# Kernel optimization log

Hardware: AMD Instinct MI355X
Metric: run time of the kernel (lower is better)

The kernel has to match this reference:

```python
import jax, jax.numpy as jnp
import numpy as np

B, N, D, CF = 8, 2048, 512, 128  # batch, nodes, feat_dim, count_feat


def setup_inputs() -> dict:
    key = jax.random.key(0)
    ks = jax.random.split(key, 12)
    s = 1.0 / np.sqrt(D)
    return {
        "X": jax.random.normal(ks[0], (B, N, D), jnp.float32),
        # first MultiHeadAttention (num_heads=1, mode='QK', out_features=feat_dim)
        "Wq1": jax.random.normal(ks[1], (D, D), jnp.float32) * s,
        "Wk1": jax.random.normal(ks[2], (D, D), jnp.float32) * s,
        "Wv1": jax.random.normal(ks[3], (D, D), jnp.float32) * s,
        "Wo1": jax.random.normal(ks[4], (D, D), jnp.float32) * s,
        # score attention (only its raw QK^T scores are used downstream)
        "Wq2": jax.random.normal(ks[5], (D, D), jnp.float32) * s,
        "Wk2": jax.random.normal(ks[6], (D, D), jnp.float32) * s,
        # count_mlp: Linear(D,CF) -> LeakyReLU(0.1) -> Linear(CF,1)
        "W1": jax.random.normal(ks[7], (D, CF), jnp.float32) * s,
        "b1": jnp.zeros((CF,), jnp.float32),
        "W2": jax.random.normal(ks[8], (CF, 1), jnp.float32) * (1.0 / np.sqrt(CF)),
        "b2": jnp.zeros((1,), jnp.float32),
    }


def reference(X, Wq1, Wk1, Wv1, Wo1, Wq2, Wk2, W1, b1, W2, b2):
    scale = 1.0 / jnp.sqrt(jnp.asarray(X.shape[-1], X.dtype))
    # --- first self-attention: att = softmax(QK^T/sqrt(d)) V Wo ---
    q1 = X @ Wq1
    k1 = X @ Wk1
    v1 = X @ Wv1
    s1 = jnp.einsum("bnd,bmd->bnm", q1, k1) * scale      # [B,N,N]
    p1 = jax.nn.softmax(s1, axis=-1)
    att = jnp.einsum("bnm,bmd->bnd", p1, v1) @ Wo1        # [B,N,D]
    # --- score attention over att: only raw scores are consumed ---
    s2 = jnp.einsum("bnd,bmd->bnm", att @ Wq2, att @ Wk2) * scale  # [B,N,N]
    # --- count_mlp threshold per node ---
    h = att @ W1 + b1
    h = jnp.where(h >= 0, h, 0.1 * h)                     # LeakyReLU(0.1)
    thresh = h @ W2 + b2                                  # [B,N,1]
    # --- mlp_score_thresh readout: clamp, row-normalize, clip ---
    surv = jnp.maximum(s2 - thresh, 0.0)                  # broadcast over last dim
    A = jnp.clip(surv / (jnp.sum(surv, axis=-1, keepdims=True) + 1e-9), 0.0, 1.0)
    return A
```

## Files before the change

### kernel.cpp

```cpp
#include <hip/hip_runtime.h>
#include <hip/hip_bf16.h>

#define BB 8
#define NN 2048
#define DD 512
#define CFF 128
#define MT (BB*NN)

typedef _Float16 half_t;
typedef __attribute__((ext_vector_type(8))) _Float16 half8;
typedef __attribute__((ext_vector_type(4))) float floatx4;
typedef __attribute__((ext_vector_type(4))) unsigned int uint4v;

#define MFMA16(a,b,c) __builtin_amdgcn_mfma_f32_16x16x32_f16((a),(b),(c),0,0,0)

template<int EPI>
__global__ __launch_bounds__(256) void gemm_f16s(
    const half_t* __restrict__ Ahi, const half_t* __restrict__ Alo, long lda, long sA,
    const half_t* __restrict__ Bhi, const half_t* __restrict__ Blo, long ldb, long sB,
    float* __restrict__ Cf, half_t* __restrict__ Chi, half_t* __restrict__ Clo,
    long ldc, long sC, long slotS,
    int K, float alpha, const float* __restrict__ bias, const float* __restrict__ tvec,
    float* __restrict__ rsum)
{
    const int gx = gridDim.x, gy = gridDim.y;
    int d = blockIdx.x + gx * (blockIdx.y + gy * blockIdx.z);
    int total = gx * gy * gridDim.z;
    int t0 = (d & 7) * (total >> 3) + (d >> 3);
    int bx = t0 % gx;
    int t1 = t0 / gx;
    int by = t1 % gy;
    int bz = t1 / gy;

    const int tid = threadIdx.x;
    const int row0 = by * 128, col0 = bx * 128;
    const long z = bz;
    const half_t* pAh = Ahi + z * sA + (long)row0 * lda;
    const half_t* pAl = Alo + z * sA + (long)row0 * lda;
    const half_t* pBh = Bhi + z * sB + (long)col0 * ldb;
    const half_t* pBl = Blo + z * sB + (long)col0 * ldb;

    __shared__ half_t lds[2][4][4096];

    const int l  = tid & 63;
    const int w  = tid >> 6;
    const int wr = w >> 1, wc = w & 1;
    const int Rw = wr * 64, Cw = wc * 64;
    const int rl = l & 15, kc = l >> 4;
    const int swz = (kc ^ ((rl >> 1) & 3)) * 8;

    floatx4 acc[4][4];
#pragma unroll
    for (int m = 0; m < 4; ++m)
#pragma unroll
        for (int n = 0; n < 4; ++n) acc[m][n] = (floatx4){0.f, 0.f, 0.f, 0.f};

    const int r0s = tid >> 2,         c0s = tid & 3;
    const int r1s = (tid + 256) >> 2, c1s = tid & 3;
    const int off0 = r0s * 32 + ((c0s ^ ((r0s >> 1) & 3)) * 8);
    const int off1 = r1s * 32 + ((c1s ^ ((r1s >> 1) & 3)) * 8);

    auto load_regs = [&](int k0, uint4v* r) {
        long ga0 = (long)r0s * lda + k0 + c0s * 8;
        long gb0 = (long)r0s * ldb + k0 + c0s * 8;
        long ga1 = (long)r1s * lda + k0 + c1s * 8;
        long gb1 = (long)r1s * ldb + k0 + c1s * 8;
        r[0] = *(const uint4v*)(pAh + ga0);
        r[1] = *(const uint4v*)(pAl + ga0);
        r[2] = *(const uint4v*)(pBh + gb0);
        r[3] = *(const uint4v*)(pBl + gb0);
        r[4] = *(const uint4v*)(pAh + ga1);
        r[5] = *(const uint4v*)(pAl + ga1);
        r[6] = *(const uint4v*)(pBh + gb1);
        r[7] = *(const uint4v*)(pBl + gb1);
    };
    auto write_lds = [&](int buf, const uint4v* r) {
        *(uint4v*)&lds[buf][0][off0] = r[0];
        *(uint4v*)&lds[buf][1][off0] = r[1];
        *(uint4v*)&lds[buf][2][off0] = r[2];
        *(uint4v*)&lds[buf][3][off0] = r[3];
        *(uint4v*)&lds[buf][0][off1] = r[4];
        *(uint4v*)&lds[buf][1][off1] = r[5];
        *(uint4v*)&lds[buf][2][off1] = r[6];
        *(uint4v*)&lds[buf][3][off1] = r[7];
    };

    const int nk = K >> 5;
    uint4v rg[8];
    load_regs(0, rg);
    write_lds(0, rg);
#pragma unroll 2
    for (int t = 0; t < nk; ++t) {
        __syncthreads();
        if (t + 1 < nk) load_regs((t + 1) << 5, rg);
        const int cur = t & 1;
        const half_t* bAh = &lds[cur][0][0];
        const half_t* bAl = &lds[cur][1][0];
        const half_t* bBh = &lds[cur][2][0];
        const half_t* bBl = &lds[cur][3][0];
        half8 af[4][2], bf[4][2];
#pragma unroll
        for (int m = 0; m < 4; ++m) {
            int off = (Rw + m * 16 + rl) * 32 + swz;
            af[m][0] = *(const half8*)(bAh + off);
            af[m][1] = *(const half8*)(bAl + off);
        }
#pragma unroll
        for (int n = 0; n < 4; ++n) {
            int off = (Cw + n * 16 + rl) * 32 + swz;
            bf[n][0] = *(const half8*)(bBh + off);
            bf[n][1] = *(const half8*)(bBl + off);
        }
        __builtin_amdgcn_s_setprio(1);
#pragma unroll
        for (int m = 0; m < 4; ++m)
#pragma unroll
            for (int n = 0; n < 4; ++n) {
                acc[m][n] = MFMA16(af[m][0], bf[n][0], acc[m][n]);
                acc[m][n] = MFMA16(af[m][1], bf[n][0], acc[m][n]);
                acc[m][n] = MFMA16(af[m][0], bf[n][1], acc[m][n]);
            }
        __builtin_amdgcn_s_setprio(0);
        if (t + 1 < nk) write_lds((t + 1) & 1, rg);
    }

    if (EPI == 0) {
#pragma unroll
        for (int m = 0; m < 4; ++m)
#pragma unroll
            for (int n = 0; n < 4; ++n) {
                int col = col0 + Cw + n * 16 + rl;
#pragma unroll
                for (int r = 0; r < 4; ++r) {
                    int row = row0 + Rw + m * 16 + kc * 4 + r;
                    Cf[z * sC + (long)row * ldc + col] = acc[m][n][r] * alpha;
                }
            }
    } else if (EPI == 1) {
#pragma unroll
        for (int m = 0; m < 4; ++m)
#pragma unroll
            for (int n = 0; n < 4; ++n) {
                int col = col0 + Cw + n * 16 + rl;
                long obase = (long)(col >> 9) * slotS + z * sC + (col & 511);
#pragma unroll
                for (int r = 0; r < 4; ++r) {
                    int row = row0 + Rw + m * 16 + kc * 4 + r;
                    long o = obase + (long)row * ldc;
                    float v = acc[m][n][r] * alpha;
                    half_t hh = (half_t)v;
                    Chi[o] = hh;
                    Clo[o] = (half_t)(v - (float)hh);
                }
            }
    } else if (EPI == 3) {
        const float* tv = tvec + z * NN;
        float* rs = rsum + z * NN;
#pragma unroll
        for (int m = 0; m < 4; ++m) {
#pragma unroll
            for (int r = 0; r < 4; ++r) {
                int row = row0 + Rw + m * 16 + kc * 4 + r;
                float tvr = tv[row];
                float partial = 0.f;
#pragma unroll
                for (int n = 0; n < 4; ++n) {
                    int col = col0 + Cw + n * 16 + rl;
                    float v = fmaxf(acc[m][n][r] * alpha - tvr, 0.f);
                    Cf[z * sC + (long)row * ldc + col] = v;
                    partial += v;
                }
                partial += __shfl_xor(partial, 1);
                partial += __shfl_xor(partial, 2);
                partial += __shfl_xor(partial, 4);
                partial += __shfl_xor(partial, 8);
                if (rl == 0) atomicAdd(&rs[row], partial);
            }
        }
    } else {
        float w2v[4], bv[4];
#pragma unroll
        for (int n = 0; n < 4; ++n) {
            int col = Cw + n * 16 + rl;
            bv[n]  = bias[col];
            w2v[n] = tvec[col];
        }
#pragma unroll
        for (int m = 0; m < 4; ++m) {
#pragma unroll
            for (int r = 0; r < 4; ++r) {
                int row = row0 + Rw + m * 16 + kc * 4 + r;
                float partial = 0.f;
#pragma unroll
                for (int n = 0; n < 4; ++n) {
                    float v = acc[m][n][r] + bv[n];
                    v = (v >= 0.f) ? v : 0.1f * v;
                    partial += v * w2v[n];
                }
                partial += __shfl_xor(partial, 1);
                partial += __shfl_xor(partial, 2);
                partial += __shfl_xor(partial, 4);
                partial += __shfl_xor(partial, 8);
                if (rl == 0) atomicAdd(&rsum[row], partial);
            }
        }
    }
}

__global__ __launch_bounds__(256) void wgemm3(
    const float* __restrict__ Wq1, const float* __restrict__ Wk1,
    const float* __restrict__ Wv1, const float* __restrict__ Wo1,
    const float* __restrict__ Wq2, const float* __restrict__ Wk2,
    float* __restrict__ T0, float* __restrict__ T1, float* __restrict__ T2)
{
    const int op = blockIdx.z;
    const float* A = (op == 0) ? Wq1 : (op == 1) ? Wv1 : Wq2;
    const float* B = (op == 0) ? Wk1 : (op == 1) ? Wo1 : Wk2;
    float* C = (op == 0) ? T0 : (op == 1) ? T1 : T2;
    const bool bt = (op != 1);

    __shared__ float As[32][65];
    __shared__ float Bs[32][65];
    const int tid = threadIdx.x;
    const int i0 = blockIdx.y * 64, j0 = blockIdx.x * 64;
    const int tx = tid & 15, ty = tid >> 4;
    float acc[4][4];
#pragma unroll
    for (int i = 0; i < 4; ++i)
#pragma unroll
        for (int j = 0; j < 4; ++j) acc[i][j] = 0.f;

    for (int k0 = 0; k0 < 512; k0 += 32) {
#pragma unroll
        for (int u = 0; u < 2; ++u) {
            int e = tid + u * 256;
            int r = e >> 3, c = (e & 7) * 4;
            float4 v = *(const float4*)(A + (long)(i0 + r) * 512 + k0 + c);
            As[c][r] = v.x; As[c + 1][r] = v.y; As[c + 2][r] = v.z; As[c + 3][r] = v.w;
        }
        if (bt) {
#pragma unroll
            for (int u = 0; u < 2; ++u) {
                int e = tid + u * 256;
                int r = e >> 3, c = (e & 7) * 4;
                float4 v = *(const float4*)(B + (long)(j0 + r) * 512 + k0 + c);
                Bs[c][r] = v.x; Bs[c + 1][r] = v.y; Bs[c + 2][r] = v.z; Bs[c + 3][r] = v.w;
            }
        } else {
#pragma unroll
            for (int u = 0; u < 2; ++u) {
                int e = tid + u * 256;
                int k = e >> 4, j = (e & 15) * 4;
                *(float4*)&Bs[k][j] = *(const float4*)(B + (long)(k0 + k) * 512 + j0 + j);
            }
        }
        __syncthreads();
#pragma unroll
        for (int kk = 0; kk < 32; ++kk) {
            float av[4], bv[4];
#pragma unroll
            for (int i = 0; i < 4; ++i) av[i] = As[kk][ty * 4 + i];
#pragma unroll
            for (int j = 0; j < 4; ++j) bv[j] = Bs[kk][tx * 4 + j];
#pragma unroll
            for (int i = 0; i < 4; ++i)
#pragma unroll
                for (int j = 0; j < 4; ++j)
                    acc[i][j] = fmaf(av[i], bv[j], acc[i][j]);
        }
        __syncthreads();
    }
#pragma unroll
    for (int i = 0; i < 4; ++i)
#pragma unroll
        for (int j = 0; j < 4; ++j)
            C[(long)(i0 + ty * 4 + i) * 512 + j0 + tx * 4 + j] = acc[i][j];
}

__device__ __forceinline__ float waveReduceMax(float v) {
#pragma unroll
    for (int o = 32; o; o >>= 1) v = fmaxf(v, __shfl_down(v, o));
    return v;
}
__device__ __forceinline__ float waveReduceSum(float v) {
#pragma unroll
    for (int o = 32; o; o >>= 1) v += __shfl_down(v, o);
    return v;
}

__global__ __launch_bounds__(256) void softmax_split_kernel(float* __restrict__ S)
{
    __shared__ float red[4];
    __shared__ float fin;
    long row = blockIdx.x;
    float* p = S + row * (long)NN;
    half_t* ph = (half_t*)p;
    half_t* pl = ph + NN;
    int t = threadIdx.x;

    float4 v0 = *reinterpret_cast<float4*>(p + t * 8);
    float4 v1 = *reinterpret_cast<float4*>(p + t * 8 + 4);

    float m = fmaxf(fmaxf(fmaxf(v0.x, v0.y), fmaxf(v0.z, v0.w)),
                    fmaxf(fmaxf(v1.x, v1.y), fmaxf(v1.z, v1.w)));
    m = waveReduceMax(m);
    if ((t & 63) == 0) red[t >> 6] = m;
    __syncthreads();
    if (t == 0) fin = fmaxf(fmaxf(red[0], red[1]), fmaxf(red[2], red[3]));
    __syncthreads();
    m = fin;

    float e[8];
    e[0] = __expf(v0.x - m); e[1] = __expf(v0.y - m); e[2] = __expf(v0.z - m); e[3] = __expf(v0.w - m);
    e[4] = __expf(v1.x - m); e[5] = __expf(v1.y - m); e[6] = __expf(v1.z - m); e[7] = __expf(v1.w - m);
    float s = ((e[0] + e[1]) + (e[2] + e[3])) + ((e[4] + e[5]) + (e[6] + e[7]));
    s = waveReduceSum(s);
    __syncthreads();
    if ((t & 63) == 0) red[t >> 6] = s;
    __syncthreads();
    if (t == 0) fin = (red[0] + red[1]) + (red[2] + red[3]);
    __syncthreads();
    float inv = 1.0f / fin;

    __syncthreads();
    half8 hv, lv;
#pragma unroll
    for (int j = 0; j < 8; ++j) {
        float pv = e[j] * inv;
        half_t hh = (half_t)pv;
        hv[j] = hh;
        lv[j] = (half_t)(pv - (float)hh);
    }
    *(half8*)(ph + t * 8) = hv;
    *(half8*)(pl + t * 8) = lv;
}

__global__ __launch_bounds__(256) void norm_kernel(float* __restrict__ S, const float* __restrict__ sums)
{
    long i = (long)blockIdx.x * 256 + threadIdx.x;
    long base = i * 8;
    long row = base >> 11;
    float inv = 1.0f / (sums[row] + 1e-9f);
    float4 v0 = *reinterpret_cast<float4*>(S + base);
    float4 v1 = *reinterpret_cast<float4*>(S + base + 4);
    v0.x = fminf(v0.x * inv, 1.0f); v0.y = fminf(v0.y * inv, 1.0f);
    v0.z = fminf(v0.z * inv, 1.0f); v0.w = fminf(v0.w * inv, 1.0f);
    v1.x = fminf(v1.x * inv, 1.0f); v1.y = fminf(v1.y * inv, 1.0f);
    v1.z = fminf(v1.z * inv, 1.0f); v1.w = fminf(v1.w * inv, 1.0f);
    *reinterpret_cast<float4*>(S + base) = v0;
    *reinterpret_cast<float4*>(S + base + 4) = v1;
}

__global__ __launch_bounds__(256) void init_aux(float* __restrict__ thresh, float* __restrict__ sums,
                                                const float* __restrict__ b2)
{
    int i = blockIdx.x * 256 + threadIdx.x;
    if (i < MT) { thresh[i] = b2[0]; sums[i] = 0.f; }
}

__global__ __launch_bounds__(256) void wprep(const float* __restrict__ W,
                                             half_t* __restrict__ Th, half_t* __restrict__ Tl,
                                             int K, int N, float mul)
{
    __shared__ float tw[32][33];
    int n0 = blockIdx.x * 32, k0 = blockIdx.y * 32;
    int c = threadIdx.x & 31, r8 = threadIdx.x >> 5;
#pragma unroll
    for (int i = 0; i < 4; ++i) {
        int r = r8 + i * 8;
        tw[r][c] = W[(long)(k0 + r) * N + n0 + c];
    }
    __syncthreads();
#pragma unroll
    for (int i = 0; i < 4; ++i) {
        int nr = r8 + i * 8;
        float v = tw[c][nr] * mul;
        half_t hh = (half_t)v;
        Th[(long)(n0 + nr) * K + k0 + c] = hh;
        Tl[(long)(n0 + nr) * K + k0 + c] = (half_t)(v - (float)hh);
    }
}

__global__ __launch_bounds__(256) void split_f32(const float* __restrict__ in,
                                                 half_t* __restrict__ hi, half_t* __restrict__ lo)
{
    long i = ((long)blockIdx.x * 256 + threadIdx.x) * 8;
    float4 a = *(const float4*)(in + i), b = *(const float4*)(in + i + 4);
    float v[8] = {a.x, a.y, a.z, a.w, b.x, b.y, b.z, b.w};
    half8 hv, lv;
#pragma unroll
    for (int j = 0; j < 8; ++j) {
        half_t hh = (half_t)v[j];
        hv[j] = hh;
        lv[j] = (half_t)(v[j] - (float)hh);
    }
    *(half8*)(hi + i) = hv;
    *(half8*)(lo + i) = lv;
}

static void launch_gemm16(hipStream_t s, int epi,
    const half_t* Ahi, const half_t* Alo, long lda, long sA,
    const half_t* Bhi, const half_t* Blo, long ldb, long sB,
    float* Cf, half_t* Chi, half_t* Clo, long ldc, long sC, long slotS,
    int M, int N, int K, int batch, float alpha,
    const float* bias, const float* tvec, float* rsum)
{
    dim3 g(N / 128, M / 128, batch), b(256, 1, 1);
    if (epi == 0)      gemm_f16s<0><<<g, b, 0, s>>>(Ahi, Alo, lda, sA, Bhi, Blo, ldb, sB, Cf, Chi, Clo, ldc, sC, slotS, K, alpha, bias, tvec, rsum);
    else if (epi == 1) gemm_f16s<1><<<g, b, 0, s>>>(Ahi, Alo, lda, sA, Bhi, Blo, ldb, sB, Cf, Chi, Clo, ldc, sC, slotS, K, alpha, bias, tvec, rsum);
    else if (epi == 3) gemm_f16s<3><<<g, b, 0, s>>>(Ahi, Alo, lda, sA, Bhi, Blo, ldb, sB, Cf, Chi, Clo, ldc, sC, slotS, K, alpha, bias, tvec, rsum);
    else               gemm_f16s<4><<<g, b, 0, s>>>(Ahi, Alo, lda, sA, Bhi, Blo, ldb, sB, Cf, Chi, Clo, ldc, sC, slotS, K, alpha, bias, tvec, rsum);
}

extern "C" void kernel_launch(void* const* d_in, const int* in_sizes, int n_in,
                              void* d_out, int out_size, void* d_ws, size_t ws_size,
                              hipStream_t stream)
{
    const float* X   = (const float*)d_in[0];
    const float* Wq1 = (const float*)d_in[1];
    const float* Wk1 = (const float*)d_in[2];
    const float* Wv1 = (const float*)d_in[3];
    const float* Wo1 = (const float*)d_in[4];
    const float* Wq2 = (const float*)d_in[5];
    const float* Wk2 = (const float*)d_in[6];
    const float* W1  = (const float*)d_in[7];
    const float* b1  = (const float*)d_in[8];
    const float* W2  = (const float*)d_in[9];
    const float* b2  = (const float*)d_in[10];

    float* out = (float*)d_out;
    const float scale = 0.044194173824159216f;
    const float WM = 8.0f, WMI = 0.125f;

    half_t* wsH = (half_t*)d_ws;
    const long U  = (long)MT * DD;
    const long WD = (long)DD * DD;
    half_t* sXh = wsH;          half_t* sXl = wsH + U;
    half_t* sBh = wsH + 2 * U;  half_t* sBl = wsH + 3 * U;
    half_t* sCh = wsH + 4 * U;  half_t* sCl = wsH + 5 * U;
    half_t* wptr = wsH + 6 * U;
    half_t* mb1h = wptr;            half_t* mb1l = mb1h + WD;
    half_t* mvoh = mb1l + WD;       half_t* mvol = mvoh + WD;
    half_t* mb2h = mvol + WD;       half_t* mb2l = mb2h + WD;
    half_t* w1h  = mb2l + WD;       half_t* w1l  = w1h + (long)DD * CFF;
    float*  T0 = (float*)(w1l + (long)DD * CFF);
    float*  T1 = T0 + WD;
    float*  T2 = T1 + WD;
    float*  thresh = T2 + WD;
    float*  sums   = thresh + MT;

    init_aux<<<dim3(64), dim3(256), 0, stream>>>(thresh, sums, b2);
    split_f32<<<dim3(4096), dim3(256), 0, stream>>>(X, sXh, sXl);
    wgemm3<<<dim3(8, 8, 3), dim3(256), 0, stream>>>(Wq1, Wk1, Wv1, Wo1, Wq2, Wk2, T0, T1, T2);
    wprep<<<dim3(16, 16), dim3(256), 0, stream>>>(T0, mb1h, mb1l, DD, DD, WM);
    wprep<<<dim3(16, 16), dim3(256), 0, stream>>>(T1, mvoh, mvol, DD, DD, WM);
    wprep<<<dim3(16, 16), dim3(256), 0, stream>>>(T2, mb2h, mb2l, DD, DD, WM);
    wprep<<<dim3(4, 16),  dim3(256), 0, stream>>>(W1, w1h, w1l, DD, CFF, 1.0f);

    launch_gemm16(stream, 1, sXh, sXl, DD, 0, mb1h, mb1l, DD, 0,
                  nullptr, sBh, sBl, DD, 0, 0, MT, DD, DD, 1, WMI, nullptr, nullptr, nullptr);

    launch_gemm16(stream, 0, sBh, sBl, DD, (long)NN * DD, sXh, sXl, DD, (long)NN * DD,
                  out, nullptr, nullptr, NN, (long)NN * NN, 0, NN, NN, DD, BB, scale, nullptr, nullptr, nullptr);

    launch_gemm16(stream, 1, mvoh, mvol, DD, 0, sXh, sXl, DD, (long)NN * DD,
                  nullptr, sBh, sBl, NN, (long)DD * NN, 512, DD, NN, DD, BB, WMI, nullptr, nullptr, nullptr);

    softmax_split_kernel<<<dim3(MT), dim3(256), 0, stream>>>(out);

    {
        const half_t* p1h = (const half_t*)d_out;
        const half_t* p1l = p1h + NN;
        launch_gemm16(stream, 1, p1h, p1l, 2 * NN, (long)NN * 2 * NN,
                      sBh, sBl, NN, (long)DD * NN,
                      nullptr, sCh, sCl, DD, (long)NN * DD, 0, NN, DD, NN, BB, 1.f, nullptr, nullptr, nullptr);
    }

    launch_gemm16(stream, 1, sCh, sCl, DD, 0, mb2h, mb2l, DD, 0,
                  nullptr, sBh, sBl, DD, 0, 0, MT, DD, DD, 1, WMI, nullptr, nullptr, nullptr);

    launch_gemm16(stream, 4, sCh, sCl, DD, 0, w1h, w1l, DD, 0,
                  nullptr, nullptr, nullptr, CFF, 0, 0, MT, CFF, DD, 1, 1.f, b1, W2, thresh);

    launch_gemm16(stream, 3, sBh, sBl, DD, (long)NN * DD, sCh, sCl, DD, (long)NN * DD,
                  out, nullptr, nullptr, NN, (long)NN * NN, 0, NN, NN, DD, BB, scale, nullptr, thresh, sums);

    norm_kernel<<<dim3(out_size / 2048), dim3(256), 0, stream>>>(out, sums);
}
```

Before: 728.1 us.

## Add 256-wide 512-thread split-f16 GEMM with XCD-aware block remap

Adds a new split-fp16 MFMA GEMM kernel using 256x256 (or 128x256) tiles, 8 waves, and a large dynamic-LDS double buffer. It also adds a block-index remap that spreads consecutive tiles across the 8 chiplet partitions. A dedicated GEMM handles the count-MLP threshold with the same remap. Every large GEMM is routed to the new kernels when the device reports at least 128KB of shared memory per block, to raise operand reuse per LDS load. In exchange the kernel uses far more registers and LDS, which limits occupancy to about one block per CU and can expose more load latency.

```diff
diff --git a/kernel.cpp b/kernel.cpp
--- a/kernel.cpp
+++ b/kernel.cpp
@@ -207,6 +207,320 @@
     }
 }
 
+template<int MF, int EPI>
+__global__ __launch_bounds__(512, 2) void gemm256(
+    const half_t* __restrict__ Ahi, const half_t* __restrict__ Alo, long lda, long sA,
+    const half_t* __restrict__ Bhi, const half_t* __restrict__ Blo, long ldb, long sB,
+    float* __restrict__ Cf, half_t* __restrict__ Chi, half_t* __restrict__ Clo,
+    long ldc, long sC, long slotS,
+    int K, float alpha, const float* __restrict__ tvec, float* __restrict__ rsum)
+{
+    constexpr int BM    = MF * 32;
+    constexpr int ATILE = BM * 32;
+    constexpr int BTILE = 256 * 32;
+    constexpr int PERBUF = 2 * ATILE + 2 * BTILE;
+    constexpr int oAh = 0, oAl = ATILE, oBh = 2 * ATILE, oBl = 2 * ATILE + BTILE;
+    constexpr int RA = (MF == 8) ? 2 : 1;
+
+    extern __shared__ half_t lds[];
+
+    const int gx = gridDim.x, gy = gridDim.y;
+    int d = blockIdx.x + gx * (blockIdx.y + gy * blockIdx.z);
+    int total = gx * gy * gridDim.z;
+    int t0 = (d & 7) * (total >> 3) + (d >> 3);
+    int bx = t0 % gx;
+    int t1 = t0 / gx;
+    int by = t1 % gy;
+    int bz = t1 / gy;
+
+    const int tid = threadIdx.x;
+    const int row0 = by * BM, col0 = bx * 256;
+    const long z = bz;
+    const half_t* pAh = Ahi + z * sA + (long)row0 * lda;
+    const half_t* pAl = Alo + z * sA + (long)row0 * lda;
+    const half_t* pBh = Bhi + z * sB + (long)col0 * ldb;
+    const half_t* pBl = Blo + z * sB + (long)col0 * ldb;
+
+    const int l  = tid & 63;
+    const int w  = tid >> 6;
+    const int wr = w >> 2, wc = w & 3;
+    const int Rw = wr * (BM / 2), Cw = wc * 64;
+    const int rl = l & 15, kc = l >> 4;
+    const int swz = (kc ^ ((rl >> 1) & 3)) * 8;
+
+    floatx4 acc[MF][4];
+#pragma unroll
+    for (int m = 0; m < MF; ++m)
+#pragma unroll
+        for (int n = 0; n < 4; ++n) acc[m][n] = (floatx4){0.f, 0.f, 0.f, 0.f};
+
+    long goffA[RA]; int loffA[RA];
+    long goffB[2];  int loffB[2];
+#pragma unroll
+    for (int u = 0; u < RA; ++u) {
+        int s = tid + u * 512; int r = s >> 2; int g = s & 3; int p = g ^ ((r >> 1) & 3);
+        goffA[u] = (long)r * lda + g * 8; loffA[u] = r * 32 + p * 8;
+    }
+#pragma unroll
+    for (int u = 0; u < 2; ++u) {
+        int s = tid + u * 512; int r = s >> 2; int g = s & 3; int p = g ^ ((r >> 1) & 3);
+        goffB[u] = (long)r * ldb + g * 8; loffB[u] = r * 32 + p * 8;
+    }
+
+    uint4v rgA[RA][2], rgB[2][2];
+    auto load_regs = [&](int k0) {
+#pragma unroll
+        for (int u = 0; u < RA; ++u) {
+            rgA[u][0] = *(const uint4v*)(pAh + goffA[u] + k0);
+            rgA[u][1] = *(const uint4v*)(pAl + goffA[u] + k0);
+        }
+#pragma unroll
+        for (int u = 0; u < 2; ++u) {
+            rgB[u][0] = *(const uint4v*)(pBh + goffB[u] + k0);
+            rgB[u][1] = *(const uint4v*)(pBl + goffB[u] + k0);
+        }
+    };
+    auto write_lds = [&](int buf) {
+        half_t* bp = lds + buf * PERBUF;
+#pragma unroll
+        for (int u = 0; u < RA; ++u) {
+            *(uint4v*)&bp[oAh + loffA[u]] = rgA[u][0];
+            *(uint4v*)&bp[oAl + loffA[u]] = rgA[u][1];
+        }
+#pragma unroll
+        for (int u = 0; u < 2; ++u) {
+            *(uint4v*)&bp[oBh + loffB[u]] = rgB[u][0];
+            *(uint4v*)&bp[oBl + loffB[u]] = rgB[u][1];
+        }
+    };
+
+    const int nk = K >> 5;
+    load_regs(0);
+    write_lds(0);
+#pragma unroll 2
+    for (int t = 0; t < nk; ++t) {
+        __syncthreads();
+        if (t + 1 < nk) load_regs((t + 1) << 5);
+        const half_t* bp = lds + (t & 1) * PERBUF;
+        half8 bf[4][2];
+#pragma unroll
+        for (int n = 0; n < 4; ++n) {
+            int off = (Cw + n * 16 + rl) * 32 + swz;
+            bf[n][0] = *(const half8*)(bp + oBh + off);
+            bf[n][1] = *(const half8*)(bp + oBl + off);
+        }
+#pragma unroll
+        for (int mp = 0; mp < MF / 2; ++mp) {
+            half8 af[2][2];
+#pragma unroll
+            for (int i = 0; i < 2; ++i) {
+                int off = (Rw + (mp * 2 + i) * 16 + rl) * 32 + swz;
+                af[i][0] = *(const half8*)(bp + oAh + off);
+                af[i][1] = *(const half8*)(bp + oAl + off);
+            }
+            __builtin_amdgcn_s_setprio(1);
+#pragma unroll
+            for (int i = 0; i < 2; ++i)
+#pragma unroll
+                for (int n = 0; n < 4; ++n) {
+                    const int m = mp * 2 + i;
+                    acc[m][n] = MFMA16(af[i][0], bf[n][0], acc[m][n]);
+                    acc[m][n] = MFMA16(af[i][1], bf[n][0], acc[m][n]);
+                    acc[m][n] = MFMA16(af[i][0], bf[n][1], acc[m][n]);
+                }
+            __builtin_amdgcn_s_setprio(0);
+        }
+        if (t + 1 < nk) write_lds((t + 1) & 1);
+    }
+
+    if (EPI == 0) {
+#pragma unroll
+        for (int m = 0; m < MF; ++m)
+#pragma unroll
+            for (int n = 0; n < 4; ++n) {
+                int col = col0 + Cw + n * 16 + rl;
+#pragma unroll
+                for (int r = 0; r < 4; ++r) {
+                    int row = row0 + Rw + m * 16 + kc * 4 + r;
+                    Cf[z * sC + (long)row * ldc + col] = acc[m][n][r] * alpha;
+                }
+            }
+    } else if (EPI == 1) {
+#pragma unroll
+        for (int m = 0; m < MF; ++m)
+#pragma unroll
+            for (int n = 0; n < 4; ++n) {
+                int col = col0 + Cw + n * 16 + rl;
+                long obase = (long)(col >> 9) * slotS + z * sC + (col & 511);
+#pragma unroll
+                for (int r = 0; r < 4; ++r) {
+                    int row = row0 + Rw + m * 16 + kc * 4 + r;
+                    long o = obase + (long)row * ldc;
+                    float v = acc[m][n][r] * alpha;
+                    half_t hh = (half_t)v;
+                    Chi[o] = hh;
+                    Clo[o] = (half_t)(v - (float)hh);
+                }
+            }
+    } else {
+        const float* tv = tvec + z * NN;
+        float* rs = rsum + z * NN;
+#pragma unroll
+        for (int m = 0; m < MF; ++m) {
+#pragma unroll
+            for (int r = 0; r < 4; ++r) {
+                int row = row0 + Rw + m * 16 + kc * 4 + r;
+                float tvr = tv[row];
+                float partial = 0.f;
+#pragma unroll
+                for (int n = 0; n < 4; ++n) {
+                    int col = col0 + Cw + n * 16 + rl;
+                    float v = fmaxf(acc[m][n][r] * alpha - tvr, 0.f);
+                    Cf[z * sC + (long)row * ldc + col] = v;
+                    partial += v;
+                }
+                partial += __shfl_xor(partial, 1);
+                partial += __shfl_xor(partial, 2);
+                partial += __shfl_xor(partial, 4);
+                partial += __shfl_xor(partial, 8);
+                if (rl == 0) atomicAdd(&rs[row], partial);
+            }
+        }
+    }
+}
+
+__global__ __launch_bounds__(256) void gemm_h(
+    const half_t* __restrict__ Ahi, const half_t* __restrict__ Alo, long lda,
+    const half_t* __restrict__ Bhi, const half_t* __restrict__ Blo, long ldb,
+    int K, const float* __restrict__ bias, const float* __restrict__ tvec,
+    float* __restrict__ rsum)
+{
+    const int gx = gridDim.x, gy = gridDim.y;
+    int d = blockIdx.x + gx * blockIdx.y;
+    int total = gx * gy;
+    int t0 = (d & 7) * (total >> 3) + (d >> 3);
+    int bx = t0 % gx;
+    int by = t0 / gx;
+
+    const int tid = threadIdx.x;
+    const int row0 = by * 128, col0 = bx * 128;
+    const half_t* pAh = Ahi + (long)row0 * lda;
+    const half_t* pAl = Alo + (long)row0 * lda;
+    const half_t* pBh = Bhi + (long)col0 * ldb;
+    const half_t* pBl = Blo + (long)col0 * ldb;
+
+    __shared__ half_t lds[2][4][4096];
+
+    const int l  = tid & 63;
+    const int w  = tid >> 6;
+    const int wr = w >> 1, wc = w & 1;
+    const int Rw = wr * 64, Cw = wc * 64;
+    const int rl = l & 15, kc = l >> 4;
+    const int swz = (kc ^ ((rl >> 1) & 3)) * 8;
+
+    floatx4 acc[4][4];
+#pragma unroll
+    for (int m = 0; m < 4; ++m)
+#pragma unroll
+        for (int n = 0; n < 4; ++n) acc[m][n] = (floatx4){0.f, 0.f, 0.f, 0.f};
+
+    const int r0s = tid >> 2,         c0s = tid & 3;
+    const int r1s = (tid + 256) >> 2, c1s = tid & 3;
+    const int off0 = r0s * 32 + ((c0s ^ ((r0s >> 1) & 3)) * 8);
+    const int off1 = r1s * 32 + ((c1s ^ ((r1s >> 1) & 3)) * 8);
+
+    auto load_regs = [&](int k0, uint4v* r) {
+        long ga0 = (long)r0s * lda + k0 + c0s * 8;
+        long gb0 = (long)r0s * ldb + k0 + c0s * 8;
+        long ga1 = (long)r1s * lda + k0 + c1s * 8;
+        long gb1 = (long)r1s * ldb + k0 + c1s * 8;
+        r[0] = *(const uint4v*)(pAh + ga0);
+        r[1] = *(const uint4v*)(pAl + ga0);
+        r[2] = *(const uint4v*)(pBh + gb0);
+        r[3] = *(const uint4v*)(pBl + gb0);
+        r[4] = *(const uint4v*)(pAh + ga1);
+        r[5] = *(const uint4v*)(pAl + ga1);
+        r[6] = *(const uint4v*)(pBh + gb1);
+        r[7] = *(const uint4v*)(pBl + gb1);
+    };
+    auto write_lds = [&](int buf, const uint4v* r) {
+        *(uint4v*)&lds[buf][0][off0] = r[0];
+        *(uint4v*)&lds[buf][1][off0] = r[1];
+        *(uint4v*)&lds[buf][2][off0] = r[2];
+        *(uint4v*)&lds[buf][3][off0] = r[3];
+        *(uint4v*)&lds[buf][0][off1] = r[4];
+        *(uint4v*)&lds[buf][1][off1] = r[5];
+        *(uint4v*)&lds[buf][2][off1] = r[6];
+        *(uint4v*)&lds[buf][3][off1] = r[7];
+    };
+
+    const int nk = K >> 5;
+    uint4v rg[8];
+    load_regs(0, rg);
+    write_lds(0, rg);
+#pragma unroll 2
+    for (int t = 0; t < nk; ++t) {
+        __syncthreads();
+        if (t + 1 < nk) load_regs((t + 1) << 5, rg);
+        const int cur = t & 1;
+        const half_t* bAh = &lds[cur][0][0];
+        const half_t* bAl = &lds[cur][1][0];
+        const half_t* bBh = &lds[cur][2][0];
+        const half_t* bBl = &lds[cur][3][0];
+        half8 af[4][2], bf[4][2];
+#pragma unroll
+        for (int m = 0; m < 4; ++m) {
+            int off = (Rw + m * 16 + rl) * 32 + swz;
+            af[m][0] = *(const half8*)(bAh + off);
+            af[m][1] = *(const half8*)(bAl + off);
+        }
+#pragma unroll
+        for (int n = 0; n < 4; ++n) {
+            int off = (Cw + n * 16 + rl) * 32 + swz;
+            bf[n][0] = *(const half8*)(bBh + off);
+            bf[n][1] = *(const half8*)(bBl + off);
+        }
+        __builtin_amdgcn_s_setprio(1);
+#pragma unroll
+        for (int m = 0; m < 4; ++m)
+#pragma unroll
+            for (int n = 0; n < 4; ++n) {
+                acc[m][n] = MFMA16(af[m][0], bf[n][0], acc[m][n]);
+                acc[m][n] = MFMA16(af[m][1], bf[n][0], acc[m][n]);
+                acc[m][n] = MFMA16(af[m][0], bf[n][1], acc[m][n]);
+            }
+        __builtin_amdgcn_s_setprio(0);
+        if (t + 1 < nk) write_lds((t + 1) & 1, rg);
+    }
+
+    float w2v[4], bv[4];
+#pragma unroll
+    for (int n = 0; n < 4; ++n) {
+        int col = Cw + n * 16 + rl;
+        bv[n]  = bias[col];
+        w2v[n] = tvec[col];
+    }
+#pragma unroll
+    for (int m = 0; m < 4; ++m) {
+#pragma unroll
+        for (int r = 0; r < 4; ++r) {
+            int row = row0 + Rw + m * 16 + kc * 4 + r;
+            float partial = 0.f;
+#pragma unroll
+            for (int n = 0; n < 4; ++n) {
+                float v = acc[m][n][r] + bv[n];
+                v = (v >= 0.f) ? v : 0.1f * v;
+                partial += v * w2v[n];
+            }
+            partial += __shfl_xor(partial, 1);
+            partial += __shfl_xor(partial, 2);
+            partial += __shfl_xor(partial, 4);
+            partial += __shfl_xor(partial, 8);
+            if (rl == 0) atomicAdd(&rsum[row], partial);
+        }
+    }
+}
+
 __global__ __launch_bounds__(256) void wgemm3(
     const float* __restrict__ Wq1, const float* __restrict__ Wk1,
     const float* __restrict__ Wv1, const float* __restrict__ Wo1,
@@ -412,6 +726,27 @@
     else               gemm_f16s<4><<<g, b, 0, s>>>(Ahi, Alo, lda, sA, Bhi, Blo, ldb, sB, Cf, Chi, Clo, ldc, sC, slotS, K, alpha, bias, tvec, rsum);
 }
 
+static void launch_g256(hipStream_t s, int mf, int epi,
+    const half_t* Ahi, const half_t* Alo, long lda, long sA,
+    const half_t* Bhi, const half_t* Blo, long ldb, long sB,
+    float* Cf, half_t* Chi, half_t* Clo, long ldc, long sC, long slotS,
+    int M, int N, int K, int batch, float alpha,
+    const float* tvec, float* rsum)
+{
+    dim3 b(512, 1, 1);
+    if (mf == 8) {
+        dim3 g(N / 256, M / 256, batch);
+        const size_t sh = 131072;
+        if (epi == 0)      gemm256<8, 0><<<g, b, sh, s>>>(Ahi, Alo, lda, sA, Bhi, Blo, ldb, sB, Cf, Chi, Clo, ldc, sC, slotS, K, alpha, tvec, rsum);
+        else if (epi == 1) gemm256<8, 1><<<g, b, sh, s>>>(Ahi, Alo, lda, sA, Bhi, Blo, ldb, sB, Cf, Chi, Clo, ldc, sC, slotS, K, alpha, tvec, rsum);
+        else               gemm256<8, 3><<<g, b, sh, s>>>(Ahi, Alo, lda, sA, Bhi, Blo, ldb, sB, Cf, Chi, Clo, ldc, sC, slotS, K, alpha, tvec, rsum);
+    } else {
+        dim3 g(N / 256, M / 128, batch);
+        const size_t sh = 98304;
+        gemm256<4, 1><<<g, b, sh, s>>>(Ahi, Alo, lda, sA, Bhi, Blo, ldb, sB, Cf, Chi, Clo, ldc, sC, slotS, K, alpha, tvec, rsum);
+    }
+}
+
 extern "C" void kernel_launch(void* const* d_in, const int* in_sizes, int n_in,
                               void* d_out, int out_size, void* d_ws, size_t ws_size,
                               hipStream_t stream)
@@ -431,6 +766,12 @@
     float* out = (float*)d_out;
     const float scale = 0.044194173824159216f;
     const float WM = 8.0f, WMI = 0.125f;
+
+    int dev = 0;
+    hipGetDevice(&dev);
+    int maxSh = 0;
+    hipDeviceGetAttribute(&maxSh, hipDeviceAttributeMaxSharedMemoryPerBlock, dev);
+    const bool big = (maxSh >= 131072);
 
     half_t* wsH = (half_t*)d_ws;
     const long U  = (long)MT * DD;
@@ -457,33 +798,46 @@
     wprep<<<dim3(16, 16), dim3(256), 0, stream>>>(T2, mb2h, mb2l, DD, DD, WM);
     wprep<<<dim3(4, 16),  dim3(256), 0, stream>>>(W1, w1h, w1l, DD, CFF, 1.0f);
 
-    launch_gemm16(stream, 1, sXh, sXl, DD, 0, mb1h, mb1l, DD, 0,
-                  nullptr, sBh, sBl, DD, 0, 0, MT, DD, DD, 1, WMI, nullptr, nullptr, nullptr);
-
-    launch_gemm16(stream, 0, sBh, sBl, DD, (long)NN * DD, sXh, sXl, DD, (long)NN * DD,
-                  out, nullptr, nullptr, NN, (long)NN * NN, 0, NN, NN, DD, BB, scale, nullptr, nullptr, nullptr);
-
-    launch_gemm16(stream, 1, mvoh, mvol, DD, 0, sXh, sXl, DD, (long)NN * DD,
-                  nullptr, sBh, sBl, NN, (long)DD * NN, 512, DD, NN, DD, BB, WMI, nullptr, nullptr, nullptr);
-
-    softmax_split_kernel<<<dim3(MT), dim3(256), 0, stream>>>(out);
-
-    {
-        const half_t* p1h = (const half_t*)d_out;
-        const half_t* p1l = p1h + NN;
+    const half_t* p1h = (const half_t*)d_out;
+    const half_t* p1l = p1h + NN;
+
+    if (big) {
+        launch_g256(stream, 8, 1, sXh, sXl, DD, 0, mb1h, mb1l, DD, 0,
+                    nullptr, sBh, sBl, DD, 0, 0, MT, DD, DD, 1, WMI, nullptr, nullptr);
+        launch_g256(stream, 8, 0, sBh, sBl, DD, (long)NN * DD, sXh, sXl, DD, (long)NN * DD,
+                    out, nullptr, nullptr, NN, (long)NN * NN, 0, NN, NN, DD, BB, scale, nullptr, nullptr);
+        launch_g256(stream, 8, 1, mvoh, mvol, DD, 0, sXh, sXl, DD, (long)NN * DD,
+                    nullptr, sBh, sBl, NN, (long)DD * NN, 512, DD, NN, DD, BB, WMI, nullptr, nullptr);
+        softmax_split_kernel<<<dim3(MT), dim3(256), 0, stream>>>(out);
+        launch_g256(stream, 4, 1, p1h, p1l, 2 * NN, (long)NN * 2 * NN,
+                    sBh, sBl, NN, (long)DD * NN,
+                    nullptr, sCh, sCl, DD, (long)NN * DD, 0, NN, DD, NN, BB, 1.f, nullptr, nullptr);
+        launch_g256(stream, 8, 1, sCh, sCl, DD, 0, mb2h, mb2l, DD, 0,
+                    nullptr, sBh, sBl, DD, 0, 0, MT, DD, DD, 1, WMI, nullptr, nullptr);
+        {
+            dim3 g(CFF / 128, MT / 128), b(256, 1, 1);
+            gemm_h<<<g, b, 0, stream>>>(sCh, sCl, DD, w1h, w1l, DD, DD, b1, W2, thresh);
+        }
+        launch_g256(stream, 8, 3, sBh, sBl, DD, (long)NN * DD, sCh, sCl, DD, (long)NN * DD,
+                    out, nullptr, nullptr, NN, (long)NN * NN, 0, NN, NN, DD, BB, scale, thresh, sums);
+    } else {
+        launch_gemm16(stream, 1, sXh, sXl, DD, 0, mb1h, mb1l, DD, 0,
+                      nullptr, sBh, sBl, DD, 0, 0, MT, DD, DD, 1, WMI, nullptr, nullptr, nullptr);
+        launch_gemm16(stream, 0, sBh, sBl, DD, (long)NN * DD, sXh, sXl, DD, (long)NN * DD,
+                      out, nullptr, nullptr, NN, (long)NN * NN, 0, NN, NN, DD, BB, scale, nullptr, nullptr, nullptr);
+        launch_gemm16(stream, 1, mvoh, mvol, DD, 0, sXh, sXl, DD, (long)NN * DD,
+                      nullptr, sBh, sBl, NN, (long)DD * NN, 512, DD, NN, DD, BB, WMI, nullptr, nullptr, nullptr);
+        softmax_split_kernel<<<dim3(MT), dim3(256), 0, stream>>>(out);
         launch_gemm16(stream, 1, p1h, p1l, 2 * NN, (long)NN * 2 * NN,
                       sBh, sBl, NN, (long)DD * NN,
                       nullptr, sCh, sCl, DD, (long)NN * DD, 0, NN, DD, NN, BB, 1.f, nullptr, nullptr, nullptr);
-    }
-
-    launch_gemm16(stream, 1, sCh, sCl, DD, 0, mb2h, mb2l, DD, 0,
-                  nullptr, sBh, sBl, DD, 0, 0, MT, DD, DD, 1, WMI, nullptr, nullptr, nullptr);
-
-    launch_gemm16(stream, 4, sCh, sCl, DD, 0, w1h, w1l, DD, 0,
-                  nullptr, nullptr, nullptr, CFF, 0, 0, MT, CFF, DD, 1, 1.f, b1, W2, thresh);
-
-    launch_gemm16(stream, 3, sBh, sBl, DD, (long)NN * DD, sCh, sCl, DD, (long)NN * DD,
-                  out, nullptr, nullptr, NN, (long)NN * NN, 0, NN, NN, DD, BB, scale, nullptr, thresh, sums);
+        launch_gemm16(stream, 1, sCh, sCl, DD, 0, mb2h, mb2l, DD, 0,
+                      nullptr, sBh, sBl, DD, 0, 0, MT, DD, DD, 1, WMI, nullptr, nullptr, nullptr);
+        launch_gemm16(stream, 4, sCh, sCl, DD, 0, w1h, w1l, DD, 0,
+                      nullptr, nullptr, nullptr, CFF, 0, 0, MT, CFF, DD, 1, 1.f, b1, W2, thresh);
+        launch_gemm16(stream, 3, sBh, sBl, DD, (long)NN * DD, sCh, sCl, DD, (long)NN * DD,
+                      out, nullptr, nullptr, NN, (long)NN * NN, 0, NN, NN, DD, BB, scale, nullptr, thresh, sums);
+    }
 
     norm_kernel<<<dim3(out_size / 2048), dim3(256), 0, stream>>>(out, sums);
 }
```

New measurement: 736.0 us. Within noise of the previous version (+1.1%).
